# Performance work log

Hardware: AMD Instinct MI355X
Metric: run time of the kernel (lower is better)

Reference implementation:

```python
import jax, jax.numpy as jnp
import numpy as np

N_NODES = 50000


def gcn_conv(x, W, b, src, dst, n_nodes):
    """PyG GCNConv: add self-loops, symmetric norm, linear, scatter-add, bias."""
    h = x @ W  # [N, out]
    # degree with self-loops: deg[i] = 1 + (# edges with dst == i)
    deg = 1.0 + jax.ops.segment_sum(jnp.ones_like(dst, dtype=h.dtype), dst,
                                    num_segments=n_nodes)
    dinv = jax.lax.rsqrt(deg)  # deg^{-1/2}
    # per-edge norm for non-self-loop edges
    norm = dinv[src] * dinv[dst]  # [E]
    agg = jax.ops.segment_sum(h[src] * norm[:, None], dst,
                              num_segments=n_nodes)
    # self-loop contribution: dinv[i]*dinv[i]*h[i] = h[i]/deg[i]
    agg = agg + h * (dinv * dinv)[:, None]
    return agg + b


def setup_inputs() -> dict:
    key = jax.random.key(0)
    ks = jax.random.split(key, 6)
    x = jax.random.normal(ks[0], (N_NODES, 512), dtype=jnp.float32)
    edge_index = jax.random.randint(ks[1], (2, 800000), 0, N_NODES,
                                    dtype=jnp.int64)
    W1 = jax.random.normal(ks[2], (512, 256), dtype=jnp.float32) * (512 ** -0.5)
    b1 = jnp.zeros((256,), dtype=jnp.float32)
    W2 = jax.random.normal(ks[3], (256, 256), dtype=jnp.float32) * (256 ** -0.5)
    b2 = jnp.zeros((256,), dtype=jnp.float32)
    W3 = jax.random.normal(ks[4], (256, 64), dtype=jnp.float32) * (256 ** -0.5)
    b3 = jnp.zeros((64,), dtype=jnp.float32)
    return {"x": x, "edge_index": edge_index, "W1": W1, "b1": b1,
            "W2": W2, "b2": b2, "W3": W3, "b3": b3}


def reference(x, edge_index, W1, b1, W2, b2, W3, b3):
    src, dst = edge_index[0], edge_index[1]
    n = x.shape[0]
    h = gcn_conv(x, W1, b1, src, dst, n)
    h = jax.nn.relu(h)  # dropout is a no-op in eval mode
    h = gcn_conv(h, W2, b2, src, dst, n)
    h = jax.nn.relu(h)
    h = gcn_conv(h, W3, b3, src, dst, n)
    # faithful to the original: softmax then log_softmax
    h = jax.nn.softmax(h, axis=1)
    return jax.nn.log_softmax(h, axis=1)
```

## Files before the change

kernel.cpp:

```cpp
#include <hip/hip_runtime.h>
#include <cstdint>
#include <cstddef>

typedef float  f32x4  __attribute__((ext_vector_type(4)));
typedef float  f32x2  __attribute__((ext_vector_type(2)));
typedef __bf16 bf16x8 __attribute__((ext_vector_type(8)));
typedef unsigned short u16x8 __attribute__((ext_vector_type(8)));

__device__ __forceinline__ unsigned short f2bf(float f) {
  union { float f; unsigned int u; } v; v.f = f;
  unsigned int r = v.u + 0x7fffu + ((v.u >> 16) & 1u);
  return (unsigned short)(r >> 16);
}
__device__ __forceinline__ unsigned int f2fp8x4(float a, float b, float c, float d) {
  int v = __builtin_amdgcn_cvt_pk_fp8_f32(a, b, 0, false);
  v = __builtin_amdgcn_cvt_pk_fp8_f32(c, d, v, true);
  return (unsigned int)v;
}
__device__ __forceinline__ unsigned char f2fp8(float f) {
  return (unsigned char)(__builtin_amdgcn_cvt_pk_fp8_f32(f, f, 0, false) & 0xff);
}
__device__ __forceinline__ void fp8x8_to_f32(uint2 d, float* f) {
  f32x2 a = __builtin_amdgcn_cvt_pk_f32_fp8((int)d.x, false);
  f32x2 b = __builtin_amdgcn_cvt_pk_f32_fp8((int)d.x, true);
  f32x2 c = __builtin_amdgcn_cvt_pk_f32_fp8((int)d.y, false);
  f32x2 e = __builtin_amdgcn_cvt_pk_f32_fp8((int)d.y, true);
  f[0] = a.x; f[1] = a.y; f[2] = b.x; f[3] = b.y;
  f[4] = c.x; f[5] = c.y; f[6] = e.x; f[7] = e.y;
}
__device__ __forceinline__ void fp8x4_to_f32(unsigned int d, float* f) {
  f32x2 a = __builtin_amdgcn_cvt_pk_f32_fp8((int)d, false);
  f32x2 b = __builtin_amdgcn_cvt_pk_f32_fp8((int)d, true);
  f[0] = a.x; f[1] = a.y; f[2] = b.x; f[3] = b.y;
}

__device__ __forceinline__ void async_copy16(const void* g, void* l) {
  __builtin_amdgcn_global_load_lds(
      (const __attribute__((address_space(1))) unsigned int*)g,
      (__attribute__((address_space(3))) unsigned int*)l, 16, 0, 0);
}

#define NN 50000
#define MPAD 50048
#define SCAN_BLOCKS 196

#define XB_BLOCKS 6256
#define WB_BLOCKS 72

__global__ void gcn_zero_k(int* __restrict__ p, int n) {
  int i = blockIdx.x * 256 + threadIdx.x;
  if (i < n) p[i] = 0;
}

__global__ void gcn_count_k(const int* __restrict__ dst, int* __restrict__ cnt, int E) {
  int e = blockIdx.x * 256 + threadIdx.x;
  if (e < E) atomicAdd(&cnt[dst[e]], 1);
}

__global__ __launch_bounds__(256) void gcn_prep_k(
    const float* __restrict__ X, unsigned char* __restrict__ x8,
    const float* __restrict__ W1, const float* __restrict__ W2,
    const float* __restrict__ W3,
    unsigned char* __restrict__ W1T8, unsigned short* __restrict__ W2T,
    unsigned short* __restrict__ W3T) {
  int b = blockIdx.x;
  if (b < XB_BLOCKS) {
    int idx16 = (b * 256 + threadIdx.x) * 16;
    int row = idx16 >> 9;
    uint4 o;
    if (row < NN) {
      const float* s = &X[idx16];
      float4 v0 = *(const float4*)s;
      float4 v1 = *(const float4*)(s + 4);
      float4 v2 = *(const float4*)(s + 8);
      float4 v3 = *(const float4*)(s + 12);
      o.x = f2fp8x4(v0.x, v0.y, v0.z, v0.w);
      o.y = f2fp8x4(v1.x, v1.y, v1.z, v1.w);
      o.z = f2fp8x4(v2.x, v2.y, v2.z, v2.w);
      o.w = f2fp8x4(v3.x, v3.y, v3.z, v3.w);
    } else {
      o = uint4{0, 0, 0, 0};
    }
    *(uint4*)&x8[idx16] = o;
  } else {
    int wb = b - XB_BLOCKS;
    if (wb < 32) {
      int idx16 = (wb * 256 + threadIdx.x) * 16;
      int n = idx16 >> 9;
      uint4 o;
      float f[16];
#pragma unroll
      for (int j = 0; j < 16; j++) {
        int k = (idx16 & 511) + j;
        f[j] = W1[(size_t)k * 256 + n];
      }
      o.x = f2fp8x4(f[0], f[1], f[2], f[3]);
      o.y = f2fp8x4(f[4], f[5], f[6], f[7]);
      o.z = f2fp8x4(f[8], f[9], f[10], f[11]);
      o.w = f2fp8x4(f[12], f[13], f[14], f[15]);
      *(uint4*)&W1T8[idx16] = o;
    } else if (wb < 64) {
      int idx8 = ((wb - 32) * 256 + threadIdx.x) * 8;
      int n = idx8 >> 8;
      u16x8 o;
#pragma unroll
      for (int j = 0; j < 8; j++) {
        int k = (idx8 & 255) + j;
        o[j] = f2bf(W2[(size_t)k * 256 + n]);
      }
      *(u16x8*)&W2T[idx8] = o;
    } else {
      int idx8 = ((wb - 64) * 256 + threadIdx.x) * 8;
      if (idx8 < 16384) {
        int n = idx8 >> 8;
        u16x8 o;
#pragma unroll
        for (int j = 0; j < 8; j++) {
          int k = (idx8 & 255) + j;
          o[j] = f2bf(W3[(size_t)k * 64 + n]);
        }
        *(u16x8*)&W3T[idx8] = o;
      }
    }
  }
}

__global__ __launch_bounds__(256) void gcn_scan_blocks_k(
    const int* __restrict__ cnt, int* __restrict__ blockSum, int nNodes) {
  __shared__ int sw[4];
  int t = threadIdx.x;
  int i = blockIdx.x * 256 + t;
  int v = (i < nNodes) ? cnt[i] : 0;
  for (int off = 32; off > 0; off >>= 1) v += __shfl_down(v, off);
  if ((t & 63) == 0) sw[t >> 6] = v;
  __syncthreads();
  if (t == 0) blockSum[blockIdx.x] = sw[0] + sw[1] + sw[2] + sw[3];
}

__global__ __launch_bounds__(256) void gcn_scan_tops_k(
    int* __restrict__ blockSum, int nBlocks) {
  __shared__ int sb[256];
  int t = threadIdx.x;
  int v = (t < nBlocks) ? blockSum[t] : 0;
  sb[t] = v;
  __syncthreads();
  for (int off = 1; off < 256; off <<= 1) {
    int x = (t >= off) ? sb[t - off] : 0;
    __syncthreads();
    sb[t] += x;
    __syncthreads();
  }
  if (t < nBlocks) blockSum[t] = sb[t] - v;
}

__global__ __launch_bounds__(256) void gcn_scan_final_k(
    const int* __restrict__ cnt, const int* __restrict__ blockSum,
    int* __restrict__ rs, int* __restrict__ cur, float* __restrict__ dinv,
    int nNodes, int E) {
  __shared__ int sb[256];
  int t = threadIdx.x;
  int i = blockIdx.x * 256 + t;
  int v = (i < nNodes) ? cnt[i] : 0;
  sb[t] = v;
  __syncthreads();
  for (int off = 1; off < 256; off <<= 1) {
    int x = (t >= off) ? sb[t - off] : 0;
    __syncthreads();
    sb[t] += x;
    __syncthreads();
  }
  if (i < nNodes) {
    int off = blockSum[blockIdx.x] + sb[t] - v;
    rs[i] = off; cur[i] = off;
    dinv[i] = rsqrtf(1.0f + (float)v);
  }
  if (i == 0) rs[nNodes] = E;
}

__global__ void gcn_scatter_k(const int* __restrict__ src, const int* __restrict__ dst,
                              int* __restrict__ cur, const float* __restrict__ dinv,
                              int2* __restrict__ e2, int E) {
  int e = blockIdx.x * 256 + threadIdx.x;
  if (e < E) {
    int d = dst[e];
    int s = src[e];
    int p = atomicAdd(&cur[d], 1);
    int2 v; v.x = s; v.y = __float_as_int(dinv[s] * dinv[d]);
    e2[p] = v;
  }
}

__global__ __launch_bounds__(256) void gcn_gemm_f8_k(
    const unsigned char* __restrict__ A8,
    const unsigned char* __restrict__ Bt8,
    unsigned char* __restrict__ C8,
    int K, int N) {
  __shared__ __align__(16) unsigned char lds_a[128 * 32];
  __shared__ __align__(16) unsigned char lds_b[128 * 32];
  const int t = threadIdx.x;
  const int wave = t >> 6, lane = t & 63;
  const int wr = wave >> 1, wc = wave & 1;
  const int quad = lane >> 4, lrow = lane & 15;
  const int m0 = blockIdx.x * 128;
  const int n0 = blockIdx.y * 128;

  f32x4 acc[4][4] = {};

  for (int k0 = 0; k0 < K; k0 += 32) {
    __syncthreads();
    {
      int r = t >> 1, c = (t & 1) * 16;
      async_copy16(&A8[(size_t)(m0 + r) * K + k0 + c], &lds_a[t * 16]);
      async_copy16(&Bt8[(size_t)(n0 + r) * K + k0 + c], &lds_b[t * 16]);
    }
    __syncthreads();
    long af[4], bfr[4];
#pragma unroll
    for (int mt = 0; mt < 4; mt++)
      af[mt] = *(const long*)&lds_a[(wr * 64 + mt * 16 + lrow) * 32 + quad * 8];
#pragma unroll
    for (int nt = 0; nt < 4; nt++)
      bfr[nt] = *(const long*)&lds_b[(wc * 64 + nt * 16 + lrow) * 32 + quad * 8];
#pragma unroll
    for (int mt = 0; mt < 4; mt++)
#pragma unroll
      for (int nt = 0; nt < 4; nt++)
        acc[mt][nt] = __builtin_amdgcn_mfma_f32_16x16x32_fp8_fp8(af[mt], bfr[nt], acc[mt][nt], 0, 0, 0);
  }

#pragma unroll
  for (int mt = 0; mt < 4; mt++)
#pragma unroll
    for (int nt = 0; nt < 4; nt++)
#pragma unroll
      for (int r = 0; r < 4; r++) {
        int row = m0 + wr * 64 + mt * 16 + quad * 4 + r;
        int col = n0 + wc * 64 + nt * 16 + lrow;
        C8[(size_t)row * N + col] = f2fp8(acc[mt][nt][r]);
      }
}

template<int BN, int WTN>
__global__ __launch_bounds__(256) void gcn_gemm_k(
    const unsigned short* __restrict__ A,
    const unsigned short* __restrict__ Bt,
    unsigned char* __restrict__ C8,
    int K, int N) {
  __shared__ __align__(16) unsigned short lds_a[128 * 32];
  __shared__ __align__(16) unsigned short lds_b[BN * 32];
  const int t = threadIdx.x;
  const int wave = t >> 6, lane = t & 63;
  const int wr = wave >> 1, wc = wave & 1;
  const int quad = lane >> 4, lrow = lane & 15;
  const int m0 = blockIdx.x * 128;
  const int n0 = blockIdx.y * BN;

  f32x4 acc[4][WTN] = {};

  for (int k0 = 0; k0 < K; k0 += 32) {
    __syncthreads();
    for (int q = t; q < 512; q += 256) {
      int r = q >> 2, c = (q & 3) * 8;
      async_copy16(&A[(size_t)(m0 + r) * K + k0 + c], &lds_a[q * 8]);
    }
    for (int q = t; q < BN * 4; q += 256) {
      int r = q >> 2, c = (q & 3) * 8;
      async_copy16(&Bt[(size_t)(n0 + r) * K + k0 + c], &lds_b[q * 8]);
    }
    __syncthreads();
    bf16x8 af[4], bfr[WTN];
#pragma unroll
    for (int mt = 0; mt < 4; mt++)
      af[mt] = *(const bf16x8*)&lds_a[(wr * 64 + mt * 16 + lrow) * 32 + quad * 8];
#pragma unroll
    for (int nt = 0; nt < WTN; nt++)
      bfr[nt] = *(const bf16x8*)&lds_b[(wc * (BN / 2) + nt * 16 + lrow) * 32 + quad * 8];
#pragma unroll
    for (int mt = 0; mt < 4; mt++)
#pragma unroll
      for (int nt = 0; nt < WTN; nt++)
        acc[mt][nt] = __builtin_amdgcn_mfma_f32_16x16x32_bf16(af[mt], bfr[nt], acc[mt][nt], 0, 0, 0);
  }

#pragma unroll
  for (int mt = 0; mt < 4; mt++)
#pragma unroll
    for (int nt = 0; nt < WTN; nt++)
#pragma unroll
      for (int r = 0; r < 4; r++) {
        int row = m0 + wr * 64 + mt * 16 + quad * 4 + r;
        int col = n0 + wc * (BN / 2) + nt * 16 + lrow;
        C8[(size_t)row * N + col] = f2fp8(acc[mt][nt][r]);
      }
}

template<int D>
__global__ __launch_bounds__(256) void gcn_agg_relu_k(
    const unsigned char* __restrict__ h8, const int* __restrict__ rs,
    const int2* __restrict__ e2, const float* __restrict__ dinv,
    const float* __restrict__ bias, unsigned short* __restrict__ out, int nNodes) {
  int wave = threadIdx.x >> 6, lane = threadIdx.x & 63;
  int i = blockIdx.x * 4 + wave;
  if (i >= nNodes) return;
  int half = lane >> 5, sub = lane & 31;
  int f0 = sub * 8;
  float di = dinv[i];
  uint2 dsel = *(const uint2*)&h8[(size_t)i * D + f0];
  float sv[8];
  fp8x8_to_f32(dsel, sv);
  float wself = (half == 0) ? di * di : 0.0f;
  float acc[8];
#pragma unroll
  for (int j = 0; j < 8; j++) acc[j] = sv[j] * wself;

  int e0 = rs[i], e1 = rs[i + 1];
  int nIter = (e1 - e0 + 7) >> 3;
  int e = e0 + half;
  for (int k = 0; k < nIter; k++) {
    int idx[4]; float w[4];
#pragma unroll
    for (int u = 0; u < 4; u++) {
      int ee = e + 2 * u;
      bool v = ee < e1;
      int2 pr = e2[v ? ee : e0];
      idx[u] = v ? pr.x : i;
      w[u] = v ? __int_as_float(pr.y) : 0.0f;
    }
    uint2 d0 = *(const uint2*)&h8[(size_t)idx[0] * D + f0];
    uint2 d1 = *(const uint2*)&h8[(size_t)idx[1] * D + f0];
    uint2 d2 = *(const uint2*)&h8[(size_t)idx[2] * D + f0];
    uint2 d3 = *(const uint2*)&h8[(size_t)idx[3] * D + f0];
    float r0[8], r1[8], r2[8], r3[8];
    fp8x8_to_f32(d0, r0); fp8x8_to_f32(d1, r1);
    fp8x8_to_f32(d2, r2); fp8x8_to_f32(d3, r3);
#pragma unroll
    for (int j = 0; j < 8; j++)
      acc[j] += r0[j] * w[0] + r1[j] * w[1] + r2[j] * w[2] + r3[j] * w[3];
    e += 8;
  }
#pragma unroll
  for (int j = 0; j < 8; j++) acc[j] += __shfl_xor(acc[j], 32);
  if (half == 0) {
    u16x8 o;
#pragma unroll
    for (int j = 0; j < 8; j++) {
      float r = acc[j] + bias[f0 + j];
      o[j] = f2bf(r > 0.0f ? r : 0.0f);
    }
    *(u16x8*)&out[(size_t)i * D + f0] = o;
  }
}

__global__ __launch_bounds__(256) void gcn_agg_final_k(
    const unsigned char* __restrict__ h8, const int* __restrict__ rs,
    const int2* __restrict__ e2, const float* __restrict__ dinv,
    const float* __restrict__ bias, float* __restrict__ out, int nNodes) {
  int wave = threadIdx.x >> 6, lane = threadIdx.x & 63;
  int i = blockIdx.x * 4 + wave;
  if (i >= nNodes) return;
  int qtr = lane >> 4, sub = lane & 15;
  int f0 = sub * 4;
  float di = dinv[i];
  unsigned int dself = *(const unsigned int*)&h8[(size_t)i * 64 + f0];
  float sv[4];
  fp8x4_to_f32(dself, sv);
  float wself = (qtr == 0) ? di * di : 0.0f;
  float acc[4];
#pragma unroll
  for (int j = 0; j < 4; j++) acc[j] = sv[j] * wself;

  int e0 = rs[i], e1 = rs[i + 1];
  int nIter = (e1 - e0 + 7) >> 3;
  int e = e0 + qtr;
  for (int k = 0; k < nIter; k++) {
    int idx[2]; float w[2];
#pragma unroll
    for (int u = 0; u < 2; u++) {
      int ee = e + 4 * u;
      bool v = ee < e1;
      int2 pr = e2[v ? ee : e0];
      idx[u] = v ? pr.x : i;
      w[u] = v ? __int_as_float(pr.y) : 0.0f;
    }
    unsigned int d0 = *(const unsigned int*)&h8[(size_t)idx[0] * 64 + f0];
    unsigned int d1 = *(const unsigned int*)&h8[(size_t)idx[1] * 64 + f0];
    float r0[4], r1[4];
    fp8x4_to_f32(d0, r0); fp8x4_to_f32(d1, r1);
#pragma unroll
    for (int j = 0; j < 4; j++)
      acc[j] += r0[j] * w[0] + r1[j] * w[1];
    e += 8;
  }
#pragma unroll
  for (int j = 0; j < 4; j++) {
    acc[j] += __shfl_xor(acc[j], 16);
    acc[j] += __shfl_xor(acc[j], 32);
    acc[j] += bias[f0 + j];
  }
  float m = fmaxf(fmaxf(acc[0], acc[1]), fmaxf(acc[2], acc[3]));
#pragma unroll
  for (int off = 8; off > 0; off >>= 1) m = fmaxf(m, __shfl_xor(m, off));
  float ex[4], s = 0.0f;
#pragma unroll
  for (int j = 0; j < 4; j++) { ex[j] = __expf(acc[j] - m); s += ex[j]; }
#pragma unroll
  for (int off = 8; off > 0; off >>= 1) s += __shfl_xor(s, off);
  float rcs = 1.0f / s;
  float p[4], s2 = 0.0f;
#pragma unroll
  for (int j = 0; j < 4; j++) { p[j] = ex[j] * rcs; s2 += __expf(p[j]); }
#pragma unroll
  for (int off = 8; off > 0; off >>= 1) s2 += __shfl_xor(s2, off);
  float ls = __logf(s2);
  if (qtr == 0) {
    float4 o; o.x = p[0] - ls; o.y = p[1] - ls; o.z = p[2] - ls; o.w = p[3] - ls;
    *(float4*)&out[(size_t)i * 64 + f0] = o;
  }
}

extern "C" void kernel_launch(void* const* d_in, const int* in_sizes, int n_in,
                              void* d_out, int out_size, void* d_ws, size_t ws_size,
                              hipStream_t stream) {
  const float* x    = (const float*)d_in[0];
  const int*   eidx = (const int*)d_in[1];
  const float* W1   = (const float*)d_in[2];
  const float* b1   = (const float*)d_in[3];
  const float* W2   = (const float*)d_in[4];
  const float* b2   = (const float*)d_in[5];
  const float* W3   = (const float*)d_in[6];
  const float* b3   = (const float*)d_in[7];
  float* out = (float*)d_out;

  const int E = in_sizes[1] / 2;
  const int* src = eidx;
  const int* dst = eidx + E;

  char* p = (char*)d_ws;
  auto alloc = [&](size_t bytes) -> void* {
    void* r = (void*)p;
    p += (bytes + 255) & ~(size_t)255;
    return r;
  };
  unsigned char*  x8   = (unsigned char*)alloc((size_t)MPAD * 512);
  unsigned char*  h8   = (unsigned char*)alloc((size_t)MPAD * 256);
  unsigned short* ab   = (unsigned short*)alloc((size_t)MPAD * 256 * 2);
  unsigned char*  h83  = (unsigned char*)alloc((size_t)MPAD * 64);
  unsigned char*  W1T8 = (unsigned char*)alloc((size_t)256 * 512);
  unsigned short* W2T  = (unsigned short*)alloc((size_t)256 * 256 * 2);
  unsigned short* W3T  = (unsigned short*)alloc((size_t)64 * 256 * 2);
  int*   cnt  = (int*)alloc((size_t)NN * 4);
  int*   rs   = (int*)alloc((size_t)(NN + 1) * 4);
  int*   cur  = (int*)alloc((size_t)NN * 4);
  float* dinv = (float*)alloc((size_t)NN * 4);
  int2*  e2   = (int2*)alloc((size_t)E * 8);
  int*   bsum = (int*)alloc((size_t)SCAN_BLOCKS * 4);

  const int EB = (E + 255) / 256;
  gcn_zero_k<<<SCAN_BLOCKS, 256, 0, stream>>>(cnt, NN);
  gcn_count_k<<<EB, 256, 0, stream>>>(dst, cnt, E);
  gcn_prep_k<<<XB_BLOCKS + WB_BLOCKS, 256, 0, stream>>>(
      x, x8, W1, W2, W3, W1T8, W2T, W3T);
  gcn_scan_blocks_k<<<SCAN_BLOCKS, 256, 0, stream>>>(cnt, bsum, NN);
  gcn_scan_tops_k<<<1, 256, 0, stream>>>(bsum, SCAN_BLOCKS);
  gcn_scan_final_k<<<SCAN_BLOCKS, 256, 0, stream>>>(cnt, bsum, rs, cur, dinv, NN, E);
  gcn_scatter_k<<<EB, 256, 0, stream>>>(src, dst, cur, dinv, e2, E);

  const int MB = MPAD / 128;
  gcn_gemm_f8_k<<<dim3(MB, 2), 256, 0, stream>>>(x8, W1T8, h8, 512, 256);
  gcn_agg_relu_k<256><<<(NN + 3) / 4, 256, 0, stream>>>(h8, rs, e2, dinv, b1, ab, NN);
  gcn_gemm_k<128, 4><<<dim3(MB, 2), 256, 0, stream>>>(ab, W2T, h8, 256, 256);
  gcn_agg_relu_k<256><<<(NN + 3) / 4, 256, 0, stream>>>(h8, rs, e2, dinv, b2, ab, NN);
  gcn_gemm_k<64, 2><<<dim3(MB, 1), 256, 0, stream>>>(ab, W3T, h83, 256, 64);
  gcn_agg_final_k<<<(NN + 3) / 4, 256, 0, stream>>>(h83, rs, e2, dinv, b3, out, NN);

  (void)n_in; (void)out_size; (void)ws_size;
}
```

Baseline: 422.5 us.

## Fuse preprocessing into persistent grid-barrier megakernel and use fp8 for all GEMMs

Merges the zeroing, degree count, input/weight conversion, three-stage scan and CSR scatter kernels into one persistent kernel of 512 blocks that synchronises with atomic grid barriers, replacing seven launches with a memset and one launch. Layers 2 and 3 now use fp8 activations and fp8 weights with fp8 MFMA instead of bf16, which halves the activation traffic between aggregation and GEMM. The grid barrier depends on all 512 blocks being resident at once, and the fp8 activations lower precision.

```diff
diff --git a/kernel.cpp b/kernel.cpp
--- a/kernel.cpp
+++ b/kernel.cpp
@@ -4,14 +4,7 @@
 
 typedef float  f32x4  __attribute__((ext_vector_type(4)));
 typedef float  f32x2  __attribute__((ext_vector_type(2)));
-typedef __bf16 bf16x8 __attribute__((ext_vector_type(8)));
-typedef unsigned short u16x8 __attribute__((ext_vector_type(8)));
-
-__device__ __forceinline__ unsigned short f2bf(float f) {
-  union { float f; unsigned int u; } v; v.f = f;
-  unsigned int r = v.u + 0x7fffu + ((v.u >> 16) & 1u);
-  return (unsigned short)(r >> 16);
-}
+
 __device__ __forceinline__ unsigned int f2fp8x4(float a, float b, float c, float d) {
   int v = __builtin_amdgcn_cvt_pk_fp8_f32(a, b, 0, false);
   v = __builtin_amdgcn_cvt_pk_fp8_f32(c, d, v, true);
@@ -43,29 +36,35 @@
 #define NN 50000
 #define MPAD 50048
 #define SCAN_BLOCKS 196
-
-#define XB_BLOCKS 6256
-#define WB_BLOCKS 72
-
-__global__ void gcn_zero_k(int* __restrict__ p, int n) {
-  int i = blockIdx.x * 256 + threadIdx.x;
-  if (i < n) p[i] = 0;
-}
-
-__global__ void gcn_count_k(const int* __restrict__ dst, int* __restrict__ cnt, int E) {
-  int e = blockIdx.x * 256 + threadIdx.x;
-  if (e < E) atomicAdd(&cnt[dst[e]], 1);
-}
-
-__global__ __launch_bounds__(256) void gcn_prep_k(
+#define MEGA_BLOCKS 512
+
+__device__ __forceinline__ void gridbar(int* bar, int idx, int nblk) {
+  __threadfence();
+  __syncthreads();
+  if (threadIdx.x == 0) {
+    __hip_atomic_fetch_add(&bar[idx], 1, __ATOMIC_RELEASE, __HIP_MEMORY_SCOPE_AGENT);
+    while (__hip_atomic_load(&bar[idx], __ATOMIC_ACQUIRE, __HIP_MEMORY_SCOPE_AGENT) < nblk) {}
+  }
+  __syncthreads();
+}
+
+__global__ __launch_bounds__(256) void gcn_mega_k(
     const float* __restrict__ X, unsigned char* __restrict__ x8,
     const float* __restrict__ W1, const float* __restrict__ W2,
     const float* __restrict__ W3,
-    unsigned char* __restrict__ W1T8, unsigned short* __restrict__ W2T,
-    unsigned short* __restrict__ W3T) {
-  int b = blockIdx.x;
-  if (b < XB_BLOCKS) {
-    int idx16 = (b * 256 + threadIdx.x) * 16;
+    unsigned char* __restrict__ W1T8, unsigned char* __restrict__ W2T8,
+    unsigned char* __restrict__ W3T8,
+    const int* __restrict__ src, const int* __restrict__ dst, int E,
+    int* __restrict__ cnt, int* __restrict__ rs, int* __restrict__ cur,
+    float* __restrict__ dinv, int2* __restrict__ e2,
+    int* __restrict__ bsum, int* __restrict__ bscan, int* __restrict__ bar) {
+  const int nb = gridDim.x;
+  const int b = blockIdx.x, t = threadIdx.x;
+  const int gtid = b * 256 + t, gstride = nb * 256;
+  __shared__ int sb[256];
+
+  for (int u = gtid; u < (MPAD * 512 / 16); u += gstride) {
+    int idx16 = u * 16;
     int row = idx16 >> 9;
     uint4 o;
     if (row < NN) {
@@ -82,106 +81,96 @@
       o = uint4{0, 0, 0, 0};
     }
     *(uint4*)&x8[idx16] = o;
-  } else {
-    int wb = b - XB_BLOCKS;
-    if (wb < 32) {
-      int idx16 = (wb * 256 + threadIdx.x) * 16;
-      int n = idx16 >> 9;
-      uint4 o;
-      float f[16];
-#pragma unroll
-      for (int j = 0; j < 16; j++) {
-        int k = (idx16 & 511) + j;
-        f[j] = W1[(size_t)k * 256 + n];
-      }
-      o.x = f2fp8x4(f[0], f[1], f[2], f[3]);
-      o.y = f2fp8x4(f[4], f[5], f[6], f[7]);
-      o.z = f2fp8x4(f[8], f[9], f[10], f[11]);
-      o.w = f2fp8x4(f[12], f[13], f[14], f[15]);
-      *(uint4*)&W1T8[idx16] = o;
-    } else if (wb < 64) {
-      int idx8 = ((wb - 32) * 256 + threadIdx.x) * 8;
-      int n = idx8 >> 8;
-      u16x8 o;
-#pragma unroll
-      for (int j = 0; j < 8; j++) {
-        int k = (idx8 & 255) + j;
-        o[j] = f2bf(W2[(size_t)k * 256 + n]);
-      }
-      *(u16x8*)&W2T[idx8] = o;
-    } else {
-      int idx8 = ((wb - 64) * 256 + threadIdx.x) * 8;
-      if (idx8 < 16384) {
-        int n = idx8 >> 8;
-        u16x8 o;
-#pragma unroll
-        for (int j = 0; j < 8; j++) {
-          int k = (idx8 & 255) + j;
-          o[j] = f2bf(W3[(size_t)k * 64 + n]);
-        }
-        *(u16x8*)&W3T[idx8] = o;
-      }
-    }
-  }
-}
-
-__global__ __launch_bounds__(256) void gcn_scan_blocks_k(
-    const int* __restrict__ cnt, int* __restrict__ blockSum, int nNodes) {
-  __shared__ int sw[4];
-  int t = threadIdx.x;
-  int i = blockIdx.x * 256 + t;
-  int v = (i < nNodes) ? cnt[i] : 0;
-  for (int off = 32; off > 0; off >>= 1) v += __shfl_down(v, off);
-  if ((t & 63) == 0) sw[t >> 6] = v;
-  __syncthreads();
-  if (t == 0) blockSum[blockIdx.x] = sw[0] + sw[1] + sw[2] + sw[3];
-}
-
-__global__ __launch_bounds__(256) void gcn_scan_tops_k(
-    int* __restrict__ blockSum, int nBlocks) {
-  __shared__ int sb[256];
-  int t = threadIdx.x;
-  int v = (t < nBlocks) ? blockSum[t] : 0;
-  sb[t] = v;
-  __syncthreads();
-  for (int off = 1; off < 256; off <<= 1) {
-    int x = (t >= off) ? sb[t - off] : 0;
+  }
+  for (int u = gtid; u < (256 * 512 / 16); u += gstride) {
+    int idx16 = u * 16;
+    int n = idx16 >> 9;
+    float f[16];
+#pragma unroll
+    for (int j = 0; j < 16; j++) f[j] = W1[(size_t)((idx16 & 511) + j) * 256 + n];
+    uint4 o;
+    o.x = f2fp8x4(f[0], f[1], f[2], f[3]);
+    o.y = f2fp8x4(f[4], f[5], f[6], f[7]);
+    o.z = f2fp8x4(f[8], f[9], f[10], f[11]);
+    o.w = f2fp8x4(f[12], f[13], f[14], f[15]);
+    *(uint4*)&W1T8[idx16] = o;
+  }
+  for (int u = gtid; u < (256 * 256 / 16); u += gstride) {
+    int idx16 = u * 16;
+    int n = idx16 >> 8;
+    float f[16];
+#pragma unroll
+    for (int j = 0; j < 16; j++) f[j] = W2[(size_t)((idx16 & 255) + j) * 256 + n];
+    uint4 o;
+    o.x = f2fp8x4(f[0], f[1], f[2], f[3]);
+    o.y = f2fp8x4(f[4], f[5], f[6], f[7]);
+    o.z = f2fp8x4(f[8], f[9], f[10], f[11]);
+    o.w = f2fp8x4(f[12], f[13], f[14], f[15]);
+    *(uint4*)&W2T8[idx16] = o;
+  }
+  for (int u = gtid; u < (64 * 256 / 16); u += gstride) {
+    int idx16 = u * 16;
+    int n = idx16 >> 8;
+    float f[16];
+#pragma unroll
+    for (int j = 0; j < 16; j++) f[j] = W3[(size_t)((idx16 & 255) + j) * 64 + n];
+    uint4 o;
+    o.x = f2fp8x4(f[0], f[1], f[2], f[3]);
+    o.y = f2fp8x4(f[4], f[5], f[6], f[7]);
+    o.z = f2fp8x4(f[8], f[9], f[10], f[11]);
+    o.w = f2fp8x4(f[12], f[13], f[14], f[15]);
+    *(uint4*)&W3T8[idx16] = o;
+  }
+
+  for (int e = gtid; e < E; e += gstride) atomicAdd(&cnt[dst[e]], 1);
+  gridbar(bar, 0, nb);
+
+  if (b < SCAN_BLOCKS) {
+    int i = b * 256 + t;
+    int v = (i < NN) ? cnt[i] : 0;
+    for (int off = 32; off > 0; off >>= 1) v += __shfl_down(v, off);
+    __shared__ int sw[4];
+    if ((t & 63) == 0) sw[t >> 6] = v;
     __syncthreads();
-    sb[t] += x;
+    if (t == 0) bsum[b] = sw[0] + sw[1] + sw[2] + sw[3];
+  }
+  gridbar(bar, 1, nb);
+
+  if (b == 0) {
+    int v = (t < SCAN_BLOCKS) ? bsum[t] : 0;
+    sb[t] = v;
     __syncthreads();
-  }
-  if (t < nBlocks) blockSum[t] = sb[t] - v;
-}
-
-__global__ __launch_bounds__(256) void gcn_scan_final_k(
-    const int* __restrict__ cnt, const int* __restrict__ blockSum,
-    int* __restrict__ rs, int* __restrict__ cur, float* __restrict__ dinv,
-    int nNodes, int E) {
-  __shared__ int sb[256];
-  int t = threadIdx.x;
-  int i = blockIdx.x * 256 + t;
-  int v = (i < nNodes) ? cnt[i] : 0;
-  sb[t] = v;
-  __syncthreads();
-  for (int off = 1; off < 256; off <<= 1) {
-    int x = (t >= off) ? sb[t - off] : 0;
+    for (int off = 1; off < 256; off <<= 1) {
+      int x = (t >= off) ? sb[t - off] : 0;
+      __syncthreads();
+      sb[t] += x;
+      __syncthreads();
+    }
+    if (t < SCAN_BLOCKS) bscan[t] = sb[t] - v;
+  }
+  gridbar(bar, 2, nb);
+
+  if (b < SCAN_BLOCKS) {
+    int i = b * 256 + t;
+    int v = (i < NN) ? cnt[i] : 0;
+    sb[t] = v;
     __syncthreads();
-    sb[t] += x;
-    __syncthreads();
-  }
-  if (i < nNodes) {
-    int off = blockSum[blockIdx.x] + sb[t] - v;
-    rs[i] = off; cur[i] = off;
-    dinv[i] = rsqrtf(1.0f + (float)v);
-  }
-  if (i == 0) rs[nNodes] = E;
-}
-
-__global__ void gcn_scatter_k(const int* __restrict__ src, const int* __restrict__ dst,
-                              int* __restrict__ cur, const float* __restrict__ dinv,
-                              int2* __restrict__ e2, int E) {
-  int e = blockIdx.x * 256 + threadIdx.x;
-  if (e < E) {
+    for (int off = 1; off < 256; off <<= 1) {
+      int x = (t >= off) ? sb[t - off] : 0;
+      __syncthreads();
+      sb[t] += x;
+      __syncthreads();
+    }
+    if (i < NN) {
+      int off = bscan[b] + sb[t] - v;
+      rs[i] = off; cur[i] = off;
+      dinv[i] = rsqrtf(1.0f + (float)v);
+    }
+    if (i == 0) rs[NN] = E;
+  }
+  gridbar(bar, 3, nb);
+
+  for (int e = gtid; e < E; e += gstride) {
     int d = dst[e];
     int s = src[e];
     int p = atomicAdd(&cur[d], 1);
@@ -190,64 +179,14 @@
   }
 }
 
+template<int BN, int WTN>
 __global__ __launch_bounds__(256) void gcn_gemm_f8_k(
     const unsigned char* __restrict__ A8,
     const unsigned char* __restrict__ Bt8,
     unsigned char* __restrict__ C8,
     int K, int N) {
   __shared__ __align__(16) unsigned char lds_a[128 * 32];
-  __shared__ __align__(16) unsigned char lds_b[128 * 32];
-  const int t = threadIdx.x;
-  const int wave = t >> 6, lane = t & 63;
-  const int wr = wave >> 1, wc = wave & 1;
-  const int quad = lane >> 4, lrow = lane & 15;
-  const int m0 = blockIdx.x * 128;
-  const int n0 = blockIdx.y * 128;
-
-  f32x4 acc[4][4] = {};
-
-  for (int k0 = 0; k0 < K; k0 += 32) {
-    __syncthreads();
-    {
-      int r = t >> 1, c = (t & 1) * 16;
-      async_copy16(&A8[(size_t)(m0 + r) * K + k0 + c], &lds_a[t * 16]);
-      async_copy16(&Bt8[(size_t)(n0 + r) * K + k0 + c], &lds_b[t * 16]);
-    }
-    __syncthreads();
-    long af[4], bfr[4];
-#pragma unroll
-    for (int mt = 0; mt < 4; mt++)
-      af[mt] = *(const long*)&lds_a[(wr * 64 + mt * 16 + lrow) * 32 + quad * 8];
-#pragma unroll
-    for (int nt = 0; nt < 4; nt++)
-      bfr[nt] = *(const long*)&lds_b[(wc * 64 + nt * 16 + lrow) * 32 + quad * 8];
-#pragma unroll
-    for (int mt = 0; mt < 4; mt++)
-#pragma unroll
-      for (int nt = 0; nt < 4; nt++)
-        acc[mt][nt] = __builtin_amdgcn_mfma_f32_16x16x32_fp8_fp8(af[mt], bfr[nt], acc[mt][nt], 0, 0, 0);
-  }
-
-#pragma unroll
-  for (int mt = 0; mt < 4; mt++)
-#pragma unroll
-    for (int nt = 0; nt < 4; nt++)
-#pragma unroll
-      for (int r = 0; r < 4; r++) {
-        int row = m0 + wr * 64 + mt * 16 + quad * 4 + r;
-        int col = n0 + wc * 64 + nt * 16 + lrow;
-        C8[(size_t)row * N + col] = f2fp8(acc[mt][nt][r]);
-      }
-}
-
-template<int BN, int WTN>
-__global__ __launch_bounds__(256) void gcn_gemm_k(
-    const unsigned short* __restrict__ A,
-    const unsigned short* __restrict__ Bt,
-    unsigned char* __restrict__ C8,
-    int K, int N) {
-  __shared__ __align__(16) unsigned short lds_a[128 * 32];
-  __shared__ __align__(16) unsigned short lds_b[BN * 32];
+  __shared__ __align__(16) unsigned char lds_b[BN * 32];
   const int t = threadIdx.x;
   const int wave = t >> 6, lane = t & 63;
   const int wr = wave >> 1, wc = wave & 1;
@@ -259,27 +198,27 @@
 
   for (int k0 = 0; k0 < K; k0 += 32) {
     __syncthreads();
-    for (int q = t; q < 512; q += 256) {
-      int r = q >> 2, c = (q & 3) * 8;
-      async_copy16(&A[(size_t)(m0 + r) * K + k0 + c], &lds_a[q * 8]);
-    }
-    for (int q = t; q < BN * 4; q += 256) {
-      int r = q >> 2, c = (q & 3) * 8;
-      async_copy16(&Bt[(size_t)(n0 + r) * K + k0 + c], &lds_b[q * 8]);
+    {
+      int r = t >> 1, c = (t & 1) * 16;
+      async_copy16(&A8[(size_t)(m0 + r) * K + k0 + c], &lds_a[t * 16]);
+    }
+    for (int q = t; q < BN * 2; q += 256) {
+      int r = q >> 1, c = (q & 1) * 16;
+      async_copy16(&Bt8[(size_t)(n0 + r) * K + k0 + c], &lds_b[q * 16]);
     }
     __syncthreads();
-    bf16x8 af[4], bfr[WTN];
+    long af[4], bfr[WTN];
 #pragma unroll
     for (int mt = 0; mt < 4; mt++)
-      af[mt] = *(const bf16x8*)&lds_a[(wr * 64 + mt * 16 + lrow) * 32 + quad * 8];
+      af[mt] = *(const long*)&lds_a[(wr * 64 + mt * 16 + lrow) * 32 + quad * 8];
 #pragma unroll
     for (int nt = 0; nt < WTN; nt++)
-      bfr[nt] = *(const bf16x8*)&lds_b[(wc * (BN / 2) + nt * 16 + lrow) * 32 + quad * 8];
+      bfr[nt] = *(const long*)&lds_b[(wc * (BN / 2) + nt * 16 + lrow) * 32 + quad * 8];
 #pragma unroll
     for (int mt = 0; mt < 4; mt++)
 #pragma unroll
       for (int nt = 0; nt < WTN; nt++)
-        acc[mt][nt] = __builtin_amdgcn_mfma_f32_16x16x32_bf16(af[mt], bfr[nt], acc[mt][nt], 0, 0, 0);
+        acc[mt][nt] = __builtin_amdgcn_mfma_f32_16x16x32_fp8_fp8(af[mt], bfr[nt], acc[mt][nt], 0, 0, 0);
   }
 
 #pragma unroll
@@ -298,7 +237,7 @@
 __global__ __launch_bounds__(256) void gcn_agg_relu_k(
     const unsigned char* __restrict__ h8, const int* __restrict__ rs,
     const int2* __restrict__ e2, const float* __restrict__ dinv,
-    const float* __restrict__ bias, unsigned short* __restrict__ out, int nNodes) {
+    const float* __restrict__ bias, unsigned char* __restrict__ out8, int nNodes) {
   int wave = threadIdx.x >> 6, lane = threadIdx.x & 63;
   int i = blockIdx.x * 4 + wave;
   if (i >= nNodes) return;
@@ -341,13 +280,16 @@
 #pragma unroll
   for (int j = 0; j < 8; j++) acc[j] += __shfl_xor(acc[j], 32);
   if (half == 0) {
-    u16x8 o;
+    float r[8];
 #pragma unroll
     for (int j = 0; j < 8; j++) {
-      float r = acc[j] + bias[f0 + j];
-      o[j] = f2bf(r > 0.0f ? r : 0.0f);
-    }
-    *(u16x8*)&out[(size_t)i * D + f0] = o;
+      float z = acc[j] + bias[f0 + j];
+      r[j] = z > 0.0f ? z : 0.0f;
+    }
+    uint2 o;
+    o.x = f2fp8x4(r[0], r[1], r[2], r[3]);
+    o.y = f2fp8x4(r[4], r[5], r[6], r[7]);
+    *(uint2*)&out8[(size_t)i * D + f0] = o;
   }
 }
 
@@ -442,36 +384,34 @@
     return r;
   };
   unsigned char*  x8   = (unsigned char*)alloc((size_t)MPAD * 512);
-  unsigned char*  h8   = (unsigned char*)alloc((size_t)MPAD * 256);
-  unsigned short* ab   = (unsigned short*)alloc((size_t)MPAD * 256 * 2);
-  unsigned char*  h83  = (unsigned char*)alloc((size_t)MPAD * 64);
+  unsigned char*  g8   = (unsigned char*)alloc((size_t)MPAD * 256);
+  unsigned char*  a8   = (unsigned char*)alloc((size_t)MPAD * 256);
+  unsigned char*  g83  = (unsigned char*)alloc((size_t)MPAD * 64);
   unsigned char*  W1T8 = (unsigned char*)alloc((size_t)256 * 512);
-  unsigned short* W2T  = (unsigned short*)alloc((size_t)256 * 256 * 2);
-  unsigned short* W3T  = (unsigned short*)alloc((size_t)64 * 256 * 2);
-  int*   cnt  = (int*)alloc((size_t)NN * 4);
+  unsigned char*  W2T8 = (unsigned char*)alloc((size_t)256 * 256);
+  unsigned char*  W3T8 = (unsigned char*)alloc((size_t)64 * 256);
+  int*   cz   = (int*)alloc((size_t)(NN + 8) * 4);
+  int*   cnt  = cz;
+  int*   bar  = cz + NN;
   int*   rs   = (int*)alloc((size_t)(NN + 1) * 4);
   int*   cur  = (int*)alloc((size_t)NN * 4);
   float* dinv = (float*)alloc((size_t)NN * 4);
   int2*  e2   = (int2*)alloc((size_t)E * 8);
-  int*   bsum = (int*)alloc((size_t)SCAN_BLOCKS * 4);
-
-  const int EB = (E + 255) / 256;
-  gcn_zero_k<<<SCAN_BLOCKS, 256, 0, stream>>>(cnt, NN);
-  gcn_count_k<<<EB, 256, 0, stream>>>(dst, cnt, E);
-  gcn_prep_k<<<XB_BLOCKS + WB_BLOCKS, 256, 0, stream>>>(
-      x, x8, W1, W2, W3, W1T8, W2T, W3T);
-  gcn_scan_blocks_k<<<SCAN_BLOCKS, 256, 0, stream>>>(cnt, bsum, NN);
-  gcn_scan_tops_k<<<1, 256, 0, stream>>>(bsum, SCAN_BLOCKS);
-  gcn_scan_final_k<<<SCAN_BLOCKS, 256, 0, stream>>>(cnt, bsum, rs, cur, dinv, NN, E);
-  gcn_scatter_k<<<EB, 256, 0, stream>>>(src, dst, cur, dinv, e2, E);
+  int*   bsum  = (int*)alloc((size_t)SCAN_BLOCKS * 4);
+  int*   bscan = (int*)alloc((size_t)SCAN_BLOCKS * 4);
+
+  hipMemsetAsync(cz, 0, (size_t)(NN + 8) * 4, stream);
+  gcn_mega_k<<<MEGA_BLOCKS, 256, 0, stream>>>(
+      x, x8, W1, W2, W3, W1T8, W2T8, W3T8,
+      src, dst, E, cnt, rs, cur, dinv, e2, bsum, bscan, bar);
 
   const int MB = MPAD / 128;
-  gcn_gemm_f8_k<<<dim3(MB, 2), 256, 0, stream>>>(x8, W1T8, h8, 512, 256);
-  gcn_agg_relu_k<256><<<(NN + 3) / 4, 256, 0, stream>>>(h8, rs, e2, dinv, b1, ab, NN);
-  gcn_gemm_k<128, 4><<<dim3(MB, 2), 256, 0, stream>>>(ab, W2T, h8, 256, 256);
-  gcn_agg_relu_k<256><<<(NN + 3) / 4, 256, 0, stream>>>(h8, rs, e2, dinv, b2, ab, NN);
-  gcn_gemm_k<64, 2><<<dim3(MB, 1), 256, 0, stream>>>(ab, W3T, h83, 256, 64);
-  gcn_agg_final_k<<<(NN + 3) / 4, 256, 0, stream>>>(h83, rs, e2, dinv, b3, out, NN);
+  gcn_gemm_f8_k<128, 4><<<dim3(MB, 2), 256, 0, stream>>>(x8, W1T8, g8, 512, 256);
+  gcn_agg_relu_k<256><<<(NN + 3) / 4, 256, 0, stream>>>(g8, rs, e2, dinv, b1, a8, NN);
+  gcn_gemm_f8_k<128, 4><<<dim3(MB, 2), 256, 0, stream>>>(a8, W2T8, g8, 256, 256);
+  gcn_agg_relu_k<256><<<(NN + 3) / 4, 256, 0, stream>>>(g8, rs, e2, dinv, b2, a8, NN);
+  gcn_gemm_f8_k<64, 2><<<dim3(MB, 1), 256, 0, stream>>>(a8, W3T8, g83, 256, 64);
+  gcn_agg_final_k<<<(NN + 3) / 4, 256, 0, stream>>>(g83, rs, e2, dinv, b3, out, NN);
 
   (void)n_in; (void)out_size; (void)ws_size;
 }
```

Result: slower. 675.9 us (+60.0%).
